# Optimization experiments

Hardware: AMD Instinct MI355X
Metric: run time of the kernel (lower is better)

The kernel has to match this reference:

```python
import jax, jax.numpy as jnp
import numpy as np

N = 8192       # batch_size
D = 128        # embedding dim
C = 1000       # num classes
EPS = 1e-8     # torch CosineSimilarity eps


def setup_inputs() -> dict:
    key = jax.random.key(0)
    k1, k2, k3, k4 = jax.random.split(key, 4)
    inst_embed = jax.random.normal(k1, (N, D), dtype=jnp.float32)
    proxy = jax.random.normal(k2, (N, D), dtype=jnp.float32)
    # binary mask marking same-class (non-negative) pairs, stored as float
    negative_mask = (jax.random.uniform(k3, (N, C)) < 0.5).astype(jnp.float32)
    labels = jax.random.randint(k4, (N,), 0, C)
    temperature = jnp.float32(0.07)
    margin = jnp.float32(0.0)
    return {
        'inst_embed': inst_embed,
        'proxy': proxy,
        'negative_mask': negative_mask,
        'labels': labels,
        'temperature': temperature,
        'margin': margin,
    }


def _remove_diag(M):
    # M: [h, h] -> [h, h-1], dropping the diagonal, row-major order (as torch bool-mask view)
    h = M.shape[0]
    j = jnp.arange(h - 1)[None, :]
    i = jnp.arange(h)[:, None]
    cols = j + (j >= i)  # skip column i in row i
    return jnp.take_along_axis(M, cols, axis=1)


def _l2_normalize(x):
    return x / jnp.maximum(jnp.linalg.norm(x, axis=-1, keepdims=True), EPS)


def reference(inst_embed, proxy, negative_mask, labels, temperature, margin):
    negative_mask = negative_mask.T                       # [C, N]
    xn = _l2_normalize(inst_embed)                        # [N, D]
    sim = xn @ xn.T                                       # [N, N] cosine similarity matrix
    instance_zone = jnp.exp((_remove_diag(sim) - margin) / temperature)  # [N, N-1]
    pn = _l2_normalize(proxy)
    inst2proxy_positive = jnp.exp((jnp.sum(xn * pn, axis=-1) - margin) / temperature)  # [N]
    # pos_collected_numerator == True branch
    mask_4_remove_negatives = _remove_diag(negative_mask[labels])        # [N, N-1]
    inst2inst_positives = instance_zone * mask_4_remove_negatives
    numerator = inst2proxy_positive + inst2inst_positives.sum(axis=1)
    denominator = inst2proxy_positive + instance_zone.sum(axis=1)
    criterion = -jnp.log(temperature * (numerator / denominator)).mean()
    return criterion
```

## Files before the change

### kernel.cpp

```cpp
#include <hip/hip_runtime.h>
#include <hip/hip_bf16.h>

typedef unsigned short u16;
typedef unsigned int   u32;
typedef unsigned long long u64;
typedef __attribute__((ext_vector_type(8))) short short8;
typedef __attribute__((ext_vector_type(4))) float float4v;

#define N 8192
#define D 128
#define C 1000
#define TILE 128
#define NW64 (N / 64)
#define JQ 4
#define GRIDY 16
#define JW (JQ * 2)
#define LOG2E 1.44269504088896340736f

__global__ void prep_kernel(const float* __restrict__ nm, u64* __restrict__ packed,
                            const float* __restrict__ x, const float* __restrict__ pr,
                            u16* __restrict__ xnb, float* __restrict__ p_out,
                            float* __restrict__ den, float* __restrict__ num,
                            const float* __restrict__ tp, const float* __restrict__ mp) {
    __shared__ u32 Ls[64 * 65];
    const int bid  = blockIdx.x;
    const int lane = threadIdx.x & 63;
    const int wv   = threadIdx.x >> 6;

    if (bid < 2048) {
        const int jt = bid & 127;
        const int lt = bid >> 7;
        const int j0 = jt * 64;
        const int l0 = lt * 64;

        if (lt < 15) {
            const int tid = threadIdx.x;
            #pragma unroll
            for (int it = 0; it < 4; it++) {
                const int r  = it * 16 + (tid >> 4);
                const int c0 = (tid & 15) * 4;
                const float4 v = *(const float4*)(nm + (size_t)(j0 + r) * C + l0 + c0);
                Ls[r * 65 + c0 + 0] = (v.x > 0.5f) ? 1u : 0u;
                Ls[r * 65 + c0 + 1] = (v.y > 0.5f) ? 1u : 0u;
                Ls[r * 65 + c0 + 2] = (v.z > 0.5f) ? 1u : 0u;
                Ls[r * 65 + c0 + 3] = (v.w > 0.5f) ? 1u : 0u;
            }
        } else {
            const int l  = l0 + lane;
            const bool lv = l < C;
            #pragma unroll
            for (int rr = 0; rr < 16; rr++) {
                const int r = wv * 16 + rr;
                float v = lv ? nm[(size_t)(j0 + r) * C + l] : 0.0f;
                Ls[r * 65 + lane] = (v > 0.5f) ? 1u : 0u;
            }
        }
        __syncthreads();
        #pragma unroll
        for (int cc = 0; cc < 16; cc++) {
            const int c = wv * 16 + cc;
            u64 m = __ballot(Ls[lane * 65 + c] != 0u);
            if (lane == 0 && (lt * 64 + c) < C)
                packed[(size_t)(lt * 64 + c) * NW64 + jt] = m;
        }
    } else {
        const int row = (bid - 2048) * 4 + wv;
        const float2* xr  = (const float2*)(x  + (size_t)row * D);
        const float2* prr = (const float2*)(pr + (size_t)row * D);
        float2 xv = xr[lane];
        float2 pv = prr[lane];

        float sx  = xv.x * xv.x + xv.y * xv.y;
        float sp  = pv.x * pv.x + pv.y * pv.y;
        float sxp = xv.x * pv.x + xv.y * pv.y;
        #pragma unroll
        for (int off = 32; off; off >>= 1) {
            sx  += __shfl_xor(sx,  off);
            sp  += __shfl_xor(sp,  off);
            sxp += __shfl_xor(sxp, off);
        }
        float nx = fmaxf(sqrtf(sx), 1e-8f);
        float np = fmaxf(sqrtf(sp), 1e-8f);
        float inv = 1.0f / nx;

        __hip_bfloat16 b0 = __float2bfloat16(xv.x * inv);
        __hip_bfloat16 b1 = __float2bfloat16(xv.y * inv);
        ((__hip_bfloat162*)xnb)[(size_t)row * 64 + lane] = __halves2bfloat162(b0, b1);

        if (lane == 0) {
            float T = tp[0], M = mp[0];
            p_out[row] = __expf((sxp / (nx * np) - M) / T);
            den[row] = 0.0f;
            num[row] = 0.0f;
        }
    }
}

#define AS1 __attribute__((address_space(1)))
#define AS3 __attribute__((address_space(3)))

static __device__ __forceinline__ void load_lds16(const u16* g, u16* l) {
    __builtin_amdgcn_global_load_lds((const AS1 u32*)(const void*)g,
                                     (AS3 u32*)(void*)l, 16, 0, 0);
}

template <bool RELOAD>
__device__ __forceinline__ void mfma_chunk(float4v (&acc)[2][2], const short8 (&a_f)[4][2],
                                           short8 (&bc)[4][2], const u16* Bnext,
                                           const int (&koff)[4]) {
    #pragma unroll
    for (int a = 0; a < 2; a++)
        #pragma unroll
        for (int b = 0; b < 2; b++)
            acc[a][b] = (float4v){0.f, 0.f, 0.f, 0.f};
    #pragma unroll
    for (int kk = 0; kk < 4; kk++) {
        #pragma unroll
        for (int tm = 0; tm < 2; tm++)
            #pragma unroll
            for (int tn = 0; tn < 2; tn++)
                acc[tm][tn] = __builtin_amdgcn_mfma_f32_16x16x32_bf16(
                    a_f[kk][tm], bc[kk][tn], acc[tm][tn], 0, 0, 0);
        if (RELOAD) {
            #pragma unroll
            for (int tn = 0; tn < 2; tn++)
                bc[kk][tn] = *(const short8*)(Bnext + tn * 2048 + koff[kk]);
        }
    }
}

template <bool DIAG, int CI>
__device__ __forceinline__ void epi_chunk(const float4v (&acc)[2][2], const u64* __restrict__ Ms,
                                          float (&dacc)[2][4], float (&nacc)[2][4],
                                          int wv, int kq, int m0,
                                          int ibase, int jbase, int q,
                                          float kA2, float kB2) {
    #pragma unroll
    for (int tm = 0; tm < 2; tm++) {
        #pragma unroll
        for (int r = 0; r < 4; r++) {
            const int lrow = wv * 32 + tm * 16 + kq * 4 + r;
            const u64 ws = Ms[lrow * JW + q * 2 + (CI >> 1)] >> m0;
            const int gi = ibase + lrow;
            #pragma unroll
            for (int tn = 0; tn < 2; tn++) {
                float e = __builtin_amdgcn_exp2f(fmaf(acc[tm][tn][r], kA2, kB2));
                if (DIAG) {
                    const int gj = jbase + CI * 32 + tn * 16 + m0;
                    if (gi == gj) e = 0.0f;
                }
                dacc[tm][r] += e;
                const u32 bit = (u32)(ws >> (((CI & 1) * 2 + tn) * 16)) & 1u;
                nacc[tm][r] = fmaf((float)bit, e, nacc[tm][r]);
            }
        }
    }
}

__global__ __launch_bounds__(256, 2)
void cc_main(const u16* __restrict__ xnb, const int* __restrict__ labels,
             const u64* __restrict__ packed,
             float* __restrict__ den, float* __restrict__ num,
             const float* __restrict__ tp, const float* __restrict__ mp) {
    __shared__ u16 Bs[TILE * D];
    __shared__ u64 Ms[TILE * JW];

    const int tid  = threadIdx.x;
    const int lane = tid & 63;
    const int wv   = tid >> 6;
    const int m0   = lane & 15;
    const int kq   = lane >> 4;
    const int ibase  = blockIdx.x * TILE;
    const int jsplit = blockIdx.y;
    const int jt0    = jsplit * JQ;

    const float T = tp[0];
    const float M = mp[0];
    const float kA2 = LOG2E / T;
    const float kB2 = -M * LOG2E / T;

    #pragma unroll
    for (int t = 0; t < 4; t++) {
        const int idx = t * 256 + tid;
        const int row = idx >> 3, h = idx & 7;
        const int lab = labels[ibase + row];
        Ms[idx] = packed[(size_t)lab * NW64 + jt0 * 2 + h];
    }

    const u16* Alane = xnb + (size_t)(ibase + wv * 32 + m0) * D + kq * 8;
    short8 a_f[4][2];
    #pragma unroll
    for (int kk = 0; kk < 4; kk++)
        #pragma unroll
        for (int tm = 0; tm < 2; tm++)
            a_f[kk][tm] = *(const short8*)(Alane + tm * (16 * D) + kk * 32);

    const int srow  = wv * 4 + (lane >> 4);
    const int sunit = (lane & 15) ^ (srow & 7);
    const u16* Bsrc = xnb + (size_t)srow * D + sunit * 8;
    u16* BsDst = (u16*)Bs + wv * 512;

    const int swz7 = m0 & 7;
    int koff[4];
    #pragma unroll
    for (int kk = 0; kk < 4; kk++) koff[kk] = ((kq + kk * 4) ^ swz7) * 8;
    const u16* LBrd = (const u16*)Bs + m0 * 128;

    float dacc[2][4] = {};
    float nacc[2][4] = {};
    float4v acc[2][2];
    short8 bc[4][2];

    for (int q = 0; q < JQ; q++) {
        const int jt = jt0 + q;
        const int jbase = jt * TILE;
        const bool diag = (jt == blockIdx.x);

        __syncthreads();
        {
            const u16* sq = Bsrc + (size_t)jbase * D;
            #pragma unroll
            for (int rnd = 0; rnd < 8; rnd++)
                load_lds16(sq + rnd * 16 * D, BsDst + rnd * 2048);
        }
        __syncthreads();

        #pragma unroll
        for (int kk = 0; kk < 4; kk++)
            #pragma unroll
            for (int tn = 0; tn < 2; tn++)
                bc[kk][tn] = *(const short8*)(LBrd + tn * 2048 + koff[kk]);

        mfma_chunk<true>(acc, a_f, bc, LBrd + 1 * 4096, koff);
        if (diag) epi_chunk<true , 0>(acc, Ms, dacc, nacc, wv, kq, m0, ibase, jbase, q, kA2, kB2);
        else      epi_chunk<false, 0>(acc, Ms, dacc, nacc, wv, kq, m0, ibase, jbase, q, kA2, kB2);

        mfma_chunk<true>(acc, a_f, bc, LBrd + 2 * 4096, koff);
        if (diag) epi_chunk<true , 1>(acc, Ms, dacc, nacc, wv, kq, m0, ibase, jbase, q, kA2, kB2);
        else      epi_chunk<false, 1>(acc, Ms, dacc, nacc, wv, kq, m0, ibase, jbase, q, kA2, kB2);

        mfma_chunk<true>(acc, a_f, bc, LBrd + 3 * 4096, koff);
        if (diag) epi_chunk<true , 2>(acc, Ms, dacc, nacc, wv, kq, m0, ibase, jbase, q, kA2, kB2);
        else      epi_chunk<false, 2>(acc, Ms, dacc, nacc, wv, kq, m0, ibase, jbase, q, kA2, kB2);

        mfma_chunk<false>(acc, a_f, bc, LBrd, koff);
        if (diag) epi_chunk<true , 3>(acc, Ms, dacc, nacc, wv, kq, m0, ibase, jbase, q, kA2, kB2);
        else      epi_chunk<false, 3>(acc, Ms, dacc, nacc, wv, kq, m0, ibase, jbase, q, kA2, kB2);
    }

    #pragma unroll
    for (int tm = 0; tm < 2; tm++) {
        #pragma unroll
        for (int r = 0; r < 4; r++) {
            float d = dacc[tm][r], n = nacc[tm][r];
            #pragma unroll
            for (int off = 1; off < 16; off <<= 1) {
                d += __shfl_xor(d, off);
                n += __shfl_xor(n, off);
            }
            if (m0 == 0) {
                const int gi = ibase + wv * 32 + tm * 16 + kq * 4 + r;
                atomicAdd(&den[gi], d);
                atomicAdd(&num[gi], n);
            }
        }
    }
}

__global__ void loss_kernel(const float* __restrict__ p, const float* __restrict__ den,
                            const float* __restrict__ num, float* __restrict__ out,
                            const float* __restrict__ tp) {
    __shared__ float red[16];
    const float T = tp[0];
    float s = 0.0f;
    #pragma unroll
    for (int t = 0; t < N / 4096; t++) {
        const int i = t * 1024 + threadIdx.x;
        const float4 pi = *(const float4*)(p   + i * 4);
        const float4 dn = *(const float4*)(den + i * 4);
        const float4 nu = *(const float4*)(num + i * 4);
        s += -__logf(T * (pi.x + nu.x) / (pi.x + dn.x));
        s += -__logf(T * (pi.y + nu.y) / (pi.y + dn.y));
        s += -__logf(T * (pi.z + nu.z) / (pi.z + dn.z));
        s += -__logf(T * (pi.w + nu.w) / (pi.w + dn.w));
    }
    #pragma unroll
    for (int off = 32; off; off >>= 1) s += __shfl_xor(s, off);
    const int lane = threadIdx.x & 63, wv = threadIdx.x >> 6;
    if (lane == 0) red[wv] = s;
    __syncthreads();
    if (wv == 0) {
        float t = (lane < 16) ? red[lane] : 0.0f;
        #pragma unroll
        for (int off = 8; off; off >>= 1) t += __shfl_xor(t, off);
        if (lane == 0) out[0] = t / (float)N;
    }
}

extern "C" void kernel_launch(void* const* d_in, const int* in_sizes, int n_in,
                              void* d_out, int out_size, void* d_ws, size_t ws_size,
                              hipStream_t stream) {
    (void)in_sizes; (void)n_in; (void)out_size; (void)ws_size;
    const float* inst   = (const float*)d_in[0];
    const float* proxy  = (const float*)d_in[1];
    const float* nm     = (const float*)d_in[2];
    const int*   labels = (const int*)d_in[3];
    const float* temp   = (const float*)d_in[4];
    const float* marg   = (const float*)d_in[5];
    float* out = (float*)d_out;

    char* ws = (char*)d_ws;
    u16*   xnb    = (u16*)ws;
    float* p_arr  = (float*)(ws + 2097152);
    u64*   packed = (u64*)(ws + 2129920);
    float* den    = (float*)(ws + 3153920);
    float* num    = (float*)(ws + 3186688);

    prep_kernel<<<4096, 256, 0, stream>>>(nm, packed, inst, proxy, xnb, p_arr,
                                          den, num, temp, marg);
    cc_main<<<dim3(N / TILE, GRIDY), 256, 0, stream>>>(xnb, labels, packed, den, num, temp, marg);
    loss_kernel<<<1, 1024, 0, stream>>>(p_arr, den, num, out, temp);
}
```

Measured before the change: 126.3 us.

## Exploit symmetry of similarity matrix to compute only upper-triangular tiles

Uses the symmetry of the cosine similarity matrix to evaluate only upper-triangular tile pairs. Each off-diagonal tile's exp values feed both the row sums for i and, through column reductions and atomics, the sums for j. The j side uses a second packed-mask lookup staged in shared memory. This roughly halves the MFMA and exp work, at the cost of extra shuffles, atomics and mask loads, plus uneven block work from the triangular decomposition.

```diff
diff --git a/kernel.cpp b/kernel.cpp
--- a/kernel.cpp
+++ b/kernel.cpp
@@ -12,9 +12,10 @@
 #define C 1000
 #define TILE 128
 #define NW64 (N / 64)
-#define JQ 4
-#define GRIDY 16
+#define NT   (N / TILE)
+#define JQ 2
 #define JW (JQ * 2)
+#define NBLKS 1056
 #define LOG2E 1.44269504088896340736f
 
 __global__ void prep_kernel(const float* __restrict__ nm, u64* __restrict__ packed,
@@ -130,11 +131,23 @@
 }
 
 template <bool DIAG, int CI>
-__device__ __forceinline__ void epi_chunk(const float4v (&acc)[2][2], const u64* __restrict__ Ms,
+__device__ __forceinline__ void epi_chunk(const float4v (&acc)[2][2],
+                                          const u64* __restrict__ Ms,
+                                          const u64* __restrict__ Ms2,
                                           float (&dacc)[2][4], float (&nacc)[2][4],
+                                          float* __restrict__ den, float* __restrict__ num,
                                           int wv, int kq, int m0,
                                           int ibase, int jbase, int q,
                                           float kA2, float kB2) {
+    float cd[2] = {0.0f, 0.0f};
+    float cn[2] = {0.0f, 0.0f};
+    u64 w2[2] = {0, 0};
+    if (!DIAG) {
+        #pragma unroll
+        for (int tn = 0; tn < 2; tn++)
+            w2[tn] = Ms2[(CI * 32 + tn * 16 + m0) * 2 + (wv >> 1)];
+    }
+    const int base2 = (wv & 1) * 32 + kq * 4;
     #pragma unroll
     for (int tm = 0; tm < 2; tm++) {
         #pragma unroll
@@ -152,6 +165,24 @@
                 dacc[tm][r] += e;
                 const u32 bit = (u32)(ws >> (((CI & 1) * 2 + tn) * 16)) & 1u;
                 nacc[tm][r] = fmaf((float)bit, e, nacc[tm][r]);
+                if (!DIAG) {
+                    cd[tn] += e;
+                    const u32 b2 = (u32)(w2[tn] >> (base2 + tm * 16 + r)) & 1u;
+                    cn[tn] = fmaf((float)b2, e, cn[tn]);
+                }
+            }
+        }
+    }
+    if (!DIAG) {
+        #pragma unroll
+        for (int tn = 0; tn < 2; tn++) {
+            float d = cd[tn], n = cn[tn];
+            d += __shfl_xor(d, 16); d += __shfl_xor(d, 32);
+            n += __shfl_xor(n, 16); n += __shfl_xor(n, 32);
+            if (kq == 0) {
+                const int gj = jbase + CI * 32 + tn * 16 + m0;
+                atomicAdd(&den[gj], d);
+                atomicAdd(&num[gj], n);
             }
         }
     }
@@ -164,15 +195,23 @@
              const float* __restrict__ tp, const float* __restrict__ mp) {
     __shared__ u16 Bs[TILE * D];
     __shared__ u64 Ms[TILE * JW];
+    __shared__ u64 Ms2[TILE * 2];
 
     const int tid  = threadIdx.x;
     const int lane = tid & 63;
     const int wv   = tid >> 6;
     const int m0   = lane & 15;
     const int kq   = lane >> 4;
-    const int ibase  = blockIdx.x * TILE;
-    const int jsplit = blockIdx.y;
-    const int jt0    = jsplit * JQ;
+
+    {
+    }
+    int brem = blockIdx.x;
+    int it = 0;
+    int nb = 32;
+    while (brem >= nb) { brem -= nb; it++; nb = (NT - it + 1) >> 1; }
+    const int jt0  = it + brem * 2;
+    const int jcnt = (NT - jt0 < 2) ? (NT - jt0) : 2;
+    const int ibase = it * TILE;
 
     const float T = tp[0];
     const float M = mp[0];
@@ -180,11 +219,12 @@
     const float kB2 = -M * LOG2E / T;
 
     #pragma unroll
-    for (int t = 0; t < 4; t++) {
+    for (int t = 0; t < 2; t++) {
         const int idx = t * 256 + tid;
-        const int row = idx >> 3, h = idx & 7;
+        const int row = idx >> 2, h = idx & 3;
+        int wd = jt0 * 2 + h; if (wd > NW64 - 1) wd = NW64 - 1;
         const int lab = labels[ibase + row];
-        Ms[idx] = packed[(size_t)lab * NW64 + jt0 * 2 + h];
+        Ms[idx] = packed[(size_t)lab * NW64 + wd];
     }
 
     const u16* Alane = xnb + (size_t)(ibase + wv * 32 + m0) * D + kq * 8;
@@ -211,10 +251,10 @@
     float4v acc[2][2];
     short8 bc[4][2];
 
-    for (int q = 0; q < JQ; q++) {
+    for (int q = 0; q < jcnt; q++) {
         const int jt = jt0 + q;
         const int jbase = jt * TILE;
-        const bool diag = (jt == blockIdx.x);
+        const bool diag = (jt == it);
 
         __syncthreads();
         {
@@ -223,6 +263,10 @@
             for (int rnd = 0; rnd < 8; rnd++)
                 load_lds16(sq + rnd * 16 * D, BsDst + rnd * 2048);
         }
+        {
+            const int jrow = jbase + (tid >> 1);
+            Ms2[tid] = packed[(size_t)labels[jrow] * NW64 + it * 2 + (tid & 1)];
+        }
         __syncthreads();
 
         #pragma unroll
@@ -232,20 +276,20 @@
                 bc[kk][tn] = *(const short8*)(LBrd + tn * 2048 + koff[kk]);
 
         mfma_chunk<true>(acc, a_f, bc, LBrd + 1 * 4096, koff);
-        if (diag) epi_chunk<true , 0>(acc, Ms, dacc, nacc, wv, kq, m0, ibase, jbase, q, kA2, kB2);
-        else      epi_chunk<false, 0>(acc, Ms, dacc, nacc, wv, kq, m0, ibase, jbase, q, kA2, kB2);
+        if (diag) epi_chunk<true , 0>(acc, Ms, Ms2, dacc, nacc, den, num, wv, kq, m0, ibase, jbase, q, kA2, kB2);
+        else      epi_chunk<false, 0>(acc, Ms, Ms2, dacc, nacc, den, num, wv, kq, m0, ibase, jbase, q, kA2, kB2);
 
         mfma_chunk<true>(acc, a_f, bc, LBrd + 2 * 4096, koff);
-        if (diag) epi_chunk<true , 1>(acc, Ms, dacc, nacc, wv, kq, m0, ibase, jbase, q, kA2, kB2);
-        else      epi_chunk<false, 1>(acc, Ms, dacc, nacc, wv, kq, m0, ibase, jbase, q, kA2, kB2);
+        if (diag) epi_chunk<true , 1>(acc, Ms, Ms2, dacc, nacc, den, num, wv, kq, m0, ibase, jbase, q, kA2, kB2);
+        else      epi_chunk<false, 1>(acc, Ms, Ms2, dacc, nacc, den, num, wv, kq, m0, ibase, jbase, q, kA2, kB2);
 
         mfma_chunk<true>(acc, a_f, bc, LBrd + 3 * 4096, koff);
-        if (diag) epi_chunk<true , 2>(acc, Ms, dacc, nacc, wv, kq, m0, ibase, jbase, q, kA2, kB2);
-        else      epi_chunk<false, 2>(acc, Ms, dacc, nacc, wv, kq, m0, ibase, jbase, q, kA2, kB2);
+        if (diag) epi_chunk<true , 2>(acc, Ms, Ms2, dacc, nacc, den, num, wv, kq, m0, ibase, jbase, q, kA2, kB2);
+        else      epi_chunk<false, 2>(acc, Ms, Ms2, dacc, nacc, den, num, wv, kq, m0, ibase, jbase, q, kA2, kB2);
 
         mfma_chunk<false>(acc, a_f, bc, LBrd, koff);
-        if (diag) epi_chunk<true , 3>(acc, Ms, dacc, nacc, wv, kq, m0, ibase, jbase, q, kA2, kB2);
-        else      epi_chunk<false, 3>(acc, Ms, dacc, nacc, wv, kq, m0, ibase, jbase, q, kA2, kB2);
+        if (diag) epi_chunk<true , 3>(acc, Ms, Ms2, dacc, nacc, den, num, wv, kq, m0, ibase, jbase, q, kA2, kB2);
+        else      epi_chunk<false, 3>(acc, Ms, Ms2, dacc, nacc, den, num, wv, kq, m0, ibase, jbase, q, kA2, kB2);
     }
 
     #pragma unroll
@@ -318,6 +362,6 @@
 
     prep_kernel<<<4096, 256, 0, stream>>>(nm, packed, inst, proxy, xnb, p_arr,
                                           den, num, temp, marg);
-    cc_main<<<dim3(N / TILE, GRIDY), 256, 0, stream>>>(xnb, labels, packed, den, num, temp, marg);
+    cc_main<<<NBLKS, 256, 0, stream>>>(xnb, labels, packed, den, num, temp, marg);
     loss_kernel<<<1, 1024, 0, stream>>>(p_arr, den, num, out, temp);
 }
```

New measurement: 138.2 us. 9.4% more time.
